# Kernel tuning notes

Hardware: AMD Instinct MI355X
Metric: run time of the kernel (lower is better)

The kernel has to match this reference:

```python
import jax, jax.numpy as jnp
import numpy as np

N, E, ET, C, H, L = 100000, 500000, 3, 128, 128, 3
LN_EPS = 1e-5
L2_EPS = 1e-12


def setup_inputs() -> dict:
    ks = jax.random.split(jax.random.key(0), 12)
    s = 0.05
    return {
        "x": jax.random.normal(ks[0], (N, C), jnp.float32),
        "edges": jax.random.randint(ks[1], (ET, 2, E), 0, N),
        "Wp": jax.random.normal(ks[2], (ET, C, C), jnp.float32) * s,
        "bp": jax.random.normal(ks[3], (ET, C), jnp.float32) * s,
        "Wl0": jax.random.normal(ks[4], (ET, C, H), jnp.float32) * s,
        "bl0": jax.random.normal(ks[5], (ET, H), jnp.float32) * s,
        "Wr0": jax.random.normal(ks[6], (ET, C, H), jnp.float32) * s,
        "Wl": jax.random.normal(ks[7], (L - 1, ET, H, H), jnp.float32) * s,
        "bl": jax.random.normal(ks[8], (L - 1, ET, H), jnp.float32) * s,
        "Wr": jax.random.normal(ks[9], (L - 1, ET, H, H), jnp.float32) * s,
        "ln_g": jnp.ones((L - 1, H), jnp.float32),
        "ln_b": jnp.zeros((L - 1, H), jnp.float32),
    }


def _mean_aggr(msg, dst, n):
    # scatter-mean of per-edge messages onto destination nodes
    summed = jax.ops.segment_sum(msg, dst, num_segments=n)
    deg = jax.ops.segment_sum(jnp.ones((dst.shape[0],), msg.dtype), dst, num_segments=n)
    return summed / jnp.maximum(deg, 1.0)[:, None]


def _sage(h, ei, Wl_, bl_, Wr_, Wp_=None, bp_=None, normalize=False):
    # PyG SAGEConv: out = lin_l(mean_{j in N(i)} h_j) + lin_r(h_i)
    src, dst = ei[0], ei[1]
    hs = jax.nn.relu(h @ Wp_ + bp_) if Wp_ is not None else h  # project=True path
    agg = _mean_aggr(hs[src], dst, h.shape[0])
    out = agg @ Wl_ + bl_ + h @ Wr_
    if normalize:
        out = out / jnp.maximum(jnp.linalg.norm(out, axis=-1, keepdims=True), L2_EPS)
    return out


def _layer_norm(h, g, b):
    mu = h.mean(-1, keepdims=True)
    var = ((h - mu) ** 2).mean(-1, keepdims=True)
    return (h - mu) / jnp.sqrt(var + LN_EPS) * g + b


def _forward(x, edges, Wp, bp, Wl0, bl0, Wr0, Wl, bl, Wr, ln_g, ln_b):
    et = edges.shape[0]
    # layer 0: project=True, normalize=True; HeteroConv mean over edge types
    h = sum(_sage(x, edges[t], Wl0[t], bl0[t], Wr0[t], Wp[t], bp[t], True)
            for t in range(et)) / et
    h = _layer_norm(jax.nn.relu(h), ln_g[0], ln_b[0])  # dropout = identity (eval)
    n_rest = Wl.shape[0]
    for l in range(n_rest):
        h = sum(_sage(h, edges[t], Wl[l, t], bl[l, t], Wr[l, t])
                for t in range(et)) / et
        if l != n_rest - 1:
            h = _layer_norm(jax.nn.relu(h), ln_g[l + 1], ln_b[l + 1])
    return h


def reference(x, edges, Wp, bp, Wl0, bl0, Wr0, Wl, bl, Wr, ln_g, ln_b):
    return _forward(x, edges, Wp, bp, Wl0, bl0, Wr0, Wl, bl, Wr, ln_g, ln_b)
```

## Files before the change

kernel.cpp:

```cpp
#include <hip/hip_runtime.h>
#include <math.h>

#define CH 128
#define ETC 3
#define LN_EPS 1e-5f

typedef unsigned short u16;
typedef unsigned int u32;
typedef __attribute__((ext_vector_type(8))) short short8;
typedef __attribute__((ext_vector_type(4))) float f32x4;

__device__ __forceinline__ u16 f2bf(float f) {
    u32 u = __float_as_uint(f);
    u += 0x7FFFu + ((u >> 16) & 1u);
    return (u16)(u >> 16);
}
__device__ __forceinline__ float bflo(u32 u) { return __uint_as_float(u << 16); }
__device__ __forceinline__ float bfhi(u32 u) { return __uint_as_float(u & 0xFFFF0000u); }

__device__ __forceinline__ f32x4 mfma16(short8 a, short8 b, f32x4 c) {
    return __builtin_amdgcn_mfma_f32_16x16x32_bf16(a, b, c, 0, 0, 0);
}
__device__ __forceinline__ short8 ld8(const u16* p) { return *(const short8*)p; }

__global__ __launch_bounds__(256) void pack_w(
    const float* __restrict__ Wp, const float* __restrict__ Wl0,
    const float* __restrict__ Wr0, const float* __restrict__ Wl,
    const float* __restrict__ Wr, const float* __restrict__ bl,
    u16* __restrict__ Bswz, float* __restrict__ bls)
{
    if (blockIdx.x == 0) {
        int l = threadIdx.x >> 7, i = threadIdx.x & 127;
        bls[threadIdx.x] = (bl[((size_t)l * ETC + 0) * CH + i] +
                            bl[((size_t)l * ETC + 1) * CH + i] +
                            bl[((size_t)l * ETC + 2) * CH + i]) * (1.f / 3.f);
    }
    int grp = blockIdx.x * 256 + threadIdx.x;
    if (grp >= 17 * 2048) return;
    int lane = grp & 63;
    int t1 = grp >> 6;
    int nt = t1 & 7, t2 = t1 >> 3;
    int s = t2 & 3, mat = t2 >> 2;
    int q = lane >> 4, c = lane & 15;
    int nn = nt * 16 + c;

    const float* s0;
    const float* s1 = nullptr;
    const float* s2 = nullptr;
    float scale = 1.f;
    if (mat < 3) {
        s0 = Wp + (size_t)mat * CH * CH;
    } else if (mat < 9) {
        int t = (mat - 3) >> 1;
        s0 = ((mat - 3) & 1) ? Wr0 + (size_t)t * CH * CH : Wl0 + (size_t)t * CH * CH;
    } else {
        int l = (mat < 13) ? 0 : 1;
        int mm = mat - (l ? 13 : 9);
        scale = 1.f / 3.f;
        if (mm < 3) s0 = Wl + ((size_t)l * ETC + mm) * CH * CH;
        else {
            s0 = Wr + ((size_t)l * ETC + 0) * CH * CH;
            s1 = s0 + CH * CH;
            s2 = s1 + CH * CH;
        }
    }
    short8 o;
    #pragma unroll
    for (int j = 0; j < 8; ++j) {
        int k = s * 32 + q * 8 + j;
        float v = s0[(size_t)k * CH + nn];
        if (s1) v += s1[(size_t)k * CH + nn] + s2[(size_t)k * CH + nn];
        o[j] = (short)f2bf(v * scale);
    }
    *(short8*)&Bswz[(size_t)grp * 8] = o;
}

__global__ __launch_bounds__(256) void cast_x(
    const float* __restrict__ x, u16* __restrict__ xb, int total)
{
    int i = (blockIdx.x * 256 + threadIdx.x) * 8;
    if (i >= total) return;
    short8 o;
    #pragma unroll
    for (int j = 0; j < 8; ++j) o[j] = (short)f2bf(x[i + j]);
    *(short8*)&xb[i] = o;
}

template<int MODE>
__global__ __launch_bounds__(256) void combine_k(
    const u16* __restrict__ agg0, const u16* __restrict__ agg1,
    const u16* __restrict__ agg2, const u16* __restrict__ self,
    const u16* __restrict__ Bs, const float* __restrict__ bias,
    const float* __restrict__ lg, const float* __restrict__ lb,
    u16* __restrict__ outb, float* __restrict__ outf, int nrows)
{
    constexpr int RF = 2;
    __shared__ __align__(16) u16 Bsh[CH * CH];
    const int tid = threadIdx.x;
    const int w = tid >> 6, lane = tid & 63;
    const int q = lane >> 4, c = lane & 15;
    const int rbase = (blockIdx.x * 4 + w) * (RF * 16);
    const u16* aggs[3] = {agg0, agg1, agg2};
    constexpr int NM = (MODE == 0) ? 6 : ((MODE == 3) ? 1 : 4);

    f32x4 acc[RF][8] = {};
    f32x4 res[RF][8];
    if constexpr (MODE == 0) {
        #pragma unroll
        for (int rf = 0; rf < RF; ++rf)
            #pragma unroll
            for (int nt = 0; nt < 8; ++nt) res[rf][nt] = (f32x4){0.f, 0.f, 0.f, 0.f};
    }

    #pragma unroll
    for (int m = 0; m < NM; ++m) {
        __syncthreads();
        const u16* bsrc = Bs + (size_t)m * CH * CH;
        #pragma unroll
        for (int i = 0; i < 8; ++i)
            *(short8*)&Bsh[(i * 256 + tid) * 8] = ld8(&bsrc[(i * 256 + tid) * 8]);
        __syncthreads();

        const u16* A;
        if constexpr (MODE == 0)      A = (m & 1) ? self : aggs[m >> 1];
        else if constexpr (MODE == 3) A = self;
        else                          A = (m < 3) ? aggs[m] : self;

        #pragma unroll
        for (int s = 0; s < 4; ++s) {
            short8 af[RF];
            #pragma unroll
            for (int rf = 0; rf < RF; ++rf)
                af[rf] = ld8(&A[(size_t)(rbase + rf * 16 + c) * CH + s * 32 + q * 8]);
            #pragma unroll
            for (int nt = 0; nt < 8; ++nt) {
                short8 bv = *(const short8*)&Bsh[((size_t)(s * 8 + nt) * 64 + lane) * 8];
                #pragma unroll
                for (int rf = 0; rf < RF; ++rf)
                    acc[rf][nt] = mfma16(af[rf], bv, acc[rf][nt]);
            }
        }

        if constexpr (MODE == 0) {
            if (m & 1) {
                const int t = m >> 1;
                #pragma unroll
                for (int rf = 0; rf < RF; ++rf) {
                    float ss[4] = {0.f, 0.f, 0.f, 0.f};
                    #pragma unroll
                    for (int nt = 0; nt < 8; ++nt) {
                        float bf = bias[t * CH + nt * 16 + c];
                        #pragma unroll
                        for (int r = 0; r < 4; ++r) {
                            float v = acc[rf][nt][r] + bf;
                            acc[rf][nt][r] = v;
                            ss[r] += v * v;
                        }
                    }
                    #pragma unroll
                    for (int msk = 1; msk < 16; msk <<= 1)
                        #pragma unroll
                        for (int r = 0; r < 4; ++r) ss[r] += __shfl_xor(ss[r], msk, 64);
                    float sc[4];
                    #pragma unroll
                    for (int r = 0; r < 4; ++r)
                        sc[r] = 1.f / (3.f * fmaxf(sqrtf(ss[r]), 1e-12f));
                    #pragma unroll
                    for (int nt = 0; nt < 8; ++nt)
                        #pragma unroll
                        for (int r = 0; r < 4; ++r) {
                            res[rf][nt][r] += acc[rf][nt][r] * sc[r];
                            acc[rf][nt][r] = 0.f;
                        }
                }
            }
        }
    }

    if constexpr (MODE != 0) {
        #pragma unroll
        for (int nt = 0; nt < 8; ++nt) {
            float bv = bias[nt * 16 + c];
            #pragma unroll
            for (int rf = 0; rf < RF; ++rf)
                #pragma unroll
                for (int r = 0; r < 4; ++r) acc[rf][nt][r] += bv;
        }
    }

    if constexpr (MODE == 2) {
        #pragma unroll
        for (int rf = 0; rf < RF; ++rf)
            #pragma unroll
            for (int nt = 0; nt < 8; ++nt)
                #pragma unroll
                for (int r = 0; r < 4; ++r) {
                    int row = rbase + rf * 16 + q * 4 + r;
                    if (row < nrows) outf[(size_t)row * CH + nt * 16 + c] = acc[rf][nt][r];
                }
        return;
    }

    if constexpr (MODE == 3) {
        #pragma unroll
        for (int rf = 0; rf < RF; ++rf)
            #pragma unroll
            for (int nt = 0; nt < 8; ++nt)
                #pragma unroll
                for (int r = 0; r < 4; ++r) {
                    int row = rbase + rf * 16 + q * 4 + r;
                    outb[(size_t)row * CH + nt * 16 + c] = f2bf(fmaxf(acc[rf][nt][r], 0.f));
                }
        return;
    }

    auto& bank = (MODE == 0) ? res : acc;
    #pragma unroll
    for (int rf = 0; rf < RF; ++rf) {
        float s1[4] = {0.f, 0.f, 0.f, 0.f}, s2[4] = {0.f, 0.f, 0.f, 0.f};
        #pragma unroll
        for (int nt = 0; nt < 8; ++nt)
            #pragma unroll
            for (int r = 0; r < 4; ++r) {
                float v = fmaxf(bank[rf][nt][r], 0.f);
                bank[rf][nt][r] = v;
                s1[r] += v;
                s2[r] += v * v;
            }
        #pragma unroll
        for (int msk = 1; msk < 16; msk <<= 1)
            #pragma unroll
            for (int r = 0; r < 4; ++r) {
                s1[r] += __shfl_xor(s1[r], msk, 64);
                s2[r] += __shfl_xor(s2[r], msk, 64);
            }
        float mu[4], rs[4];
        #pragma unroll
        for (int r = 0; r < 4; ++r) {
            mu[r] = s1[r] * (1.f / 128.f);
            float var = s2[r] * (1.f / 128.f) - mu[r] * mu[r];
            rs[r] = rsqrtf(var + LN_EPS);
        }
        #pragma unroll
        for (int nt = 0; nt < 8; ++nt) {
            float gv = lg[nt * 16 + c], bv = lb[nt * 16 + c];
            #pragma unroll
            for (int r = 0; r < 4; ++r) {
                int row = rbase + rf * 16 + q * 4 + r;
                outb[(size_t)row * CH + nt * 16 + c] =
                    f2bf((bank[rf][nt][r] - mu[r]) * rs[r] * gv + bv);
            }
        }
    }
}

__global__ __launch_bounds__(256) void agg_k(
    const u16* __restrict__ msg, const int* __restrict__ rowptr,
    const int* __restrict__ col, u16* __restrict__ agg, int n,
    int Ecap, unsigned long long aggstride)
{
    const int t = blockIdx.y;
    rowptr += (size_t)t * (n + 1);
    col += (size_t)t * Ecap;
    agg += (size_t)t * aggstride;

    int gid = blockIdx.x * 256 + threadIdx.x;
    int node = gid >> 5;
    int lane = threadIdx.x & 31;
    if (node >= n) return;
    int s = rowptr[node], e = rowptr[node + 1];
    const uint2* m64 = (const uint2*)msg;
    float a0 = 0.f, a1 = 0.f, a2 = 0.f, a3 = 0.f;
    float b0 = 0.f, b1 = 0.f, b2 = 0.f, b3 = 0.f;
    float c0 = 0.f, c1 = 0.f, c2 = 0.f, c3 = 0.f;
    float d0 = 0.f, d1 = 0.f, d2 = 0.f, d3 = 0.f;
    int j = s;
    for (; j + 4 <= e; j += 4) {
        int i0 = col[j], i1 = col[j + 1], i2 = col[j + 2], i3 = col[j + 3];
        uint2 v0 = m64[(size_t)i0 * 32 + lane];
        uint2 v1 = m64[(size_t)i1 * 32 + lane];
        uint2 v2 = m64[(size_t)i2 * 32 + lane];
        uint2 v3 = m64[(size_t)i3 * 32 + lane];
        a0 += bflo(v0.x); a1 += bfhi(v0.x); a2 += bflo(v0.y); a3 += bfhi(v0.y);
        b0 += bflo(v1.x); b1 += bfhi(v1.x); b2 += bflo(v1.y); b3 += bfhi(v1.y);
        c0 += bflo(v2.x); c1 += bfhi(v2.x); c2 += bflo(v2.y); c3 += bfhi(v2.y);
        d0 += bflo(v3.x); d1 += bfhi(v3.x); d2 += bflo(v3.y); d3 += bfhi(v3.y);
    }
    for (; j < e; ++j) {
        int i0 = col[j];
        uint2 v0 = m64[(size_t)i0 * 32 + lane];
        a0 += bflo(v0.x); a1 += bfhi(v0.x); a2 += bflo(v0.y); a3 += bfhi(v0.y);
    }
    a0 += b0 + c0 + d0; a1 += b1 + c1 + d1; a2 += b2 + c2 + d2; a3 += b3 + c3 + d3;
    float inv = 1.f / (float)max(e - s, 1);
    uint2 o;
    o.x = (u32)f2bf(a0 * inv) | ((u32)f2bf(a1 * inv) << 16);
    o.y = (u32)f2bf(a2 * inv) | ((u32)f2bf(a3 * inv) << 16);
    ((uint2*)agg)[(size_t)node * 32 + lane] = o;
}

__global__ __launch_bounds__(256) void hist_k(
    const int* __restrict__ edges, int* __restrict__ cnt, int E, int n)
{
    int t = blockIdx.y;
    int e = blockIdx.x * 256 + threadIdx.x;
    if (e >= E) return;
    int dst = edges[(size_t)t * 2 * E + E + e];
    atomicAdd(&cnt[t * n + dst], 1);
}

__global__ __launch_bounds__(256) void scan1_k(
    const int* __restrict__ cnt, int* __restrict__ bsum, int n, int nbs)
{
    int t = blockIdx.y, b = blockIdx.x;
    int i = b * 256 + threadIdx.x;
    int v = (i < n) ? cnt[t * n + i] : 0;
    #pragma unroll
    for (int m = 1; m < 64; m <<= 1) v += __shfl_xor(v, m, 64);
    __shared__ int wsum[4];
    if ((threadIdx.x & 63) == 0) wsum[threadIdx.x >> 6] = v;
    __syncthreads();
    if (threadIdx.x == 0) bsum[t * nbs + b] = wsum[0] + wsum[1] + wsum[2] + wsum[3];
}

__global__ __launch_bounds__(512) void scan2_k(int* __restrict__ bsum, int nbs, int nb)
{
    int t = blockIdx.x;
    int tid = threadIdx.x;
    __shared__ int sh[512];
    int v = (tid < nb) ? bsum[t * nbs + tid] : 0;
    sh[tid] = v;
    __syncthreads();
    for (int off = 1; off < 512; off <<= 1) {
        int x = (tid >= off) ? sh[tid - off] : 0;
        __syncthreads();
        sh[tid] += x;
        __syncthreads();
    }
    if (tid < nb) bsum[t * nbs + tid] = sh[tid] - v;
}

__global__ __launch_bounds__(256) void scan3_k(
    const int* __restrict__ cnt, const int* __restrict__ bsum,
    int* __restrict__ rowptr, int n, int nbs)
{
    int t = blockIdx.y, b = blockIdx.x;
    int tid = threadIdx.x;
    int i = b * 256 + tid;
    __shared__ int sh[256];
    int v = (i < n) ? cnt[t * n + i] : 0;
    sh[tid] = v;
    __syncthreads();
    for (int off = 1; off < 256; off <<= 1) {
        int x = (tid >= off) ? sh[tid - off] : 0;
        __syncthreads();
        sh[tid] += x;
        __syncthreads();
    }
    int excl = sh[tid] - v + bsum[t * nbs + b];
    if (i < n) rowptr[(size_t)t * (n + 1) + i] = excl;
    if (i == n - 1) rowptr[(size_t)t * (n + 1) + n] = excl + v;
}

__global__ __launch_bounds__(256) void fill_k(
    const int* __restrict__ edges, const int* __restrict__ rowptr,
    int* __restrict__ cnt2, int* __restrict__ colbuf, int E, int n)
{
    int t = blockIdx.y;
    int e = blockIdx.x * 256 + threadIdx.x;
    if (e >= E) return;
    int src = edges[(size_t)t * 2 * E + e];
    int dst = edges[(size_t)t * 2 * E + E + e];
    int pos = rowptr[(size_t)t * (n + 1) + dst] + atomicAdd(&cnt2[t * n + dst], 1);
    colbuf[(size_t)t * E + pos] = src;
}

extern "C" void kernel_launch(void* const* d_in, const int* in_sizes, int n_in,
                              void* d_out, int out_size, void* d_ws, size_t ws_size,
                              hipStream_t stream) {
    const float* x    = (const float*)d_in[0];
    const int*   edges= (const int*)d_in[1];
    const float* Wp   = (const float*)d_in[2];
    const float* bp   = (const float*)d_in[3];
    const float* Wl0  = (const float*)d_in[4];
    const float* bl0  = (const float*)d_in[5];
    const float* Wr0  = (const float*)d_in[6];
    const float* Wl   = (const float*)d_in[7];
    const float* bl   = (const float*)d_in[8];
    const float* Wr   = (const float*)d_in[9];
    const float* ln_g = (const float*)d_in[10];
    const float* ln_b = (const float*)d_in[11];
    float* out = (float*)d_out;

    const int n  = in_sizes[0] / CH;
    const int E  = in_sizes[1] / (2 * ETC);
    const int npad = ((n + 127) / 128) * 128;
    const int NBS = 512;
    const int nb = (n + 255) / 256;
    const size_t MS = (size_t)CH * CH;

    char* p = (char*)d_ws;
    u16* xb   = (u16*)p;  p += (size_t)npad * CH * 2;
    u16* hs   = (u16*)p;  p += (size_t)npad * CH * 2;
    u16* agg  = (u16*)p;  p += (size_t)ETC * npad * CH * 2;
    u16* Bswz = (u16*)p;  p += 17 * MS * 2;
    float* bls = (float*)p; p += 256 * 4;
    int* cnt    = (int*)p;  p += (size_t)ETC * n * 4;
    int* rowptr = (int*)p;  p += (size_t)ETC * (n + 1) * 4;
    int* colbuf = (int*)p;  p += (size_t)ETC * E * 4;
    int* bsum   = (int*)p;

    const dim3 b256(256);
    const dim3 ge((E + 255) / 256, ETC);
    const dim3 gs(nb, ETC);
    const int gb = (n + 127) / 128;
    const int ga = (n * 32 + 255) / 256;

    hipMemsetAsync(cnt, 0, (size_t)ETC * n * sizeof(int), stream);
    hist_k<<<ge, b256, 0, stream>>>(edges, cnt, E, n);
    scan1_k<<<gs, b256, 0, stream>>>(cnt, bsum, n, NBS);
    scan2_k<<<ETC, 512, 0, stream>>>(bsum, NBS, nb);
    scan3_k<<<gs, b256, 0, stream>>>(cnt, bsum, rowptr, n, NBS);
    hipMemsetAsync(cnt, 0, (size_t)ETC * n * sizeof(int), stream);
    fill_k<<<ge, b256, 0, stream>>>(edges, rowptr, cnt, colbuf, E, n);

    pack_w<<<136, b256, 0, stream>>>(Wp, Wl0, Wr0, Wl, Wr, bl, Bswz, bls);
    cast_x<<<(n * CH / 8 + 255) / 256, b256, 0, stream>>>(x, xb, n * CH);

    for (int t = 0; t < ETC; ++t) {
        combine_k<3><<<gb, b256, 0, stream>>>(
            nullptr, nullptr, nullptr, xb, Bswz + (size_t)t * MS, bp + t * CH,
            nullptr, nullptr, hs, nullptr, n);
        agg_k<<<dim3(ga, 1), b256, 0, stream>>>(hs, rowptr + (size_t)t * (n + 1),
                                                colbuf + (size_t)t * E,
                                                agg + (size_t)t * npad * CH, n, 0, 0ull);
    }
    combine_k<0><<<gb, b256, 0, stream>>>(agg, agg + (size_t)npad * CH,
                                          agg + (size_t)2 * npad * CH, xb,
                                          Bswz + 3 * MS, bl0, ln_g, ln_b, hs, nullptr, n);

    agg_k<<<dim3(ga, ETC), b256, 0, stream>>>(hs, rowptr, colbuf, agg, n, E,
                                              (unsigned long long)npad * CH);
    combine_k<1><<<gb, b256, 0, stream>>>(agg, agg + (size_t)npad * CH,
                                          agg + (size_t)2 * npad * CH, hs,
                                          Bswz + 9 * MS, bls, ln_g + CH, ln_b + CH,
                                          hs, nullptr, n);

    agg_k<<<dim3(ga, ETC), b256, 0, stream>>>(hs, rowptr, colbuf, agg, n, E,
                                              (unsigned long long)npad * CH);
    combine_k<2><<<gb, b256, 0, stream>>>(agg, agg + (size_t)npad * CH,
                                          agg + (size_t)2 * npad * CH, hs,
                                          Bswz + 13 * MS, bls + CH, nullptr, nullptr,
                                          nullptr, out, n);
}
```

Measured before the change: 706.2 us.

## Transform node features before aggregation and batch all edge types per launch

Uses the linearity of mean aggregation to apply the per-edge-type lin_l weights before the gather. One GEMM kernel now produces all three transformed projections plus the summed self term into a 512-wide buffer, and a single gather launch aggregates all edge types. Layer 0 also merges the three per-type projection and aggregation passes into batched launches, folds the x cast into the GEMM, and moves bias, LayerNorm and the final sum into a lightweight per-node merge kernel. This cuts kernel launches and separate per-type passes. In exchange it adds a wider intermediate buffer, strided gathers over 1 KB rows, and bf16 rounding before aggregation rather than after.

```diff
diff --git a/kernel.cpp b/kernel.cpp
--- a/kernel.cpp
+++ b/kernel.cpp
@@ -4,6 +4,7 @@
 #define CH 128
 #define ETC 3
 #define LN_EPS 1e-5f
+#define MS (CH * CH)
 
 typedef unsigned short u16;
 typedef unsigned int u32;
@@ -49,19 +50,19 @@
     const float* s2 = nullptr;
     float scale = 1.f;
     if (mat < 3) {
-        s0 = Wp + (size_t)mat * CH * CH;
+        s0 = Wp + (size_t)mat * MS;
     } else if (mat < 9) {
         int t = (mat - 3) >> 1;
-        s0 = ((mat - 3) & 1) ? Wr0 + (size_t)t * CH * CH : Wl0 + (size_t)t * CH * CH;
+        s0 = ((mat - 3) & 1) ? Wr0 + (size_t)t * MS : Wl0 + (size_t)t * MS;
     } else {
         int l = (mat < 13) ? 0 : 1;
         int mm = mat - (l ? 13 : 9);
         scale = 1.f / 3.f;
-        if (mm < 3) s0 = Wl + ((size_t)l * ETC + mm) * CH * CH;
+        if (mm < 3) s0 = Wl + ((size_t)l * ETC + mm) * MS;
         else {
-            s0 = Wr + ((size_t)l * ETC + 0) * CH * CH;
-            s1 = s0 + CH * CH;
-            s2 = s1 + CH * CH;
+            s0 = Wr + ((size_t)l * ETC + 0) * MS;
+            s1 = s0 + MS;
+            s2 = s1 + MS;
         }
     }
     short8 o;
@@ -75,212 +76,191 @@
     *(short8*)&Bswz[(size_t)grp * 8] = o;
 }
 
-__global__ __launch_bounds__(256) void cast_x(
-    const float* __restrict__ x, u16* __restrict__ xb, int total)
-{
-    int i = (blockIdx.x * 256 + threadIdx.x) * 8;
-    if (i >= total) return;
-    short8 o;
-    #pragma unroll
-    for (int j = 0; j < 8; ++j) o[j] = (short)f2bf(x[i + j]);
-    *(short8*)&xb[i] = o;
-}
-
-template<int MODE>
-__global__ __launch_bounds__(256) void combine_k(
-    const u16* __restrict__ agg0, const u16* __restrict__ agg1,
-    const u16* __restrict__ agg2, const u16* __restrict__ self,
-    const u16* __restrict__ Bs, const float* __restrict__ bias,
-    const float* __restrict__ lg, const float* __restrict__ lb,
-    u16* __restrict__ outb, float* __restrict__ outf, int nrows)
-{
-    constexpr int RF = 2;
-    __shared__ __align__(16) u16 Bsh[CH * CH];
+template<int NC, bool AF32, bool BIASRELU>
+__global__ __launch_bounds__(256) void mega_k(
+    const void* __restrict__ Ap, const u16* __restrict__ Bs,
+    const float* __restrict__ bias, u16* __restrict__ out, int nrows)
+{
+    __shared__ __align__(16) u16 Bsh[MS];
     const int tid = threadIdx.x;
     const int w = tid >> 6, lane = tid & 63;
-    const int q = lane >> 4, c = lane & 15;
-    const int rbase = (blockIdx.x * 4 + w) * (RF * 16);
-    const u16* aggs[3] = {agg0, agg1, agg2};
-    constexpr int NM = (MODE == 0) ? 6 : ((MODE == 3) ? 1 : 4);
-
-    f32x4 acc[RF][8] = {};
-    f32x4 res[RF][8];
-    if constexpr (MODE == 0) {
-        #pragma unroll
-        for (int rf = 0; rf < RF; ++rf)
-            #pragma unroll
-            for (int nt = 0; nt < 8; ++nt) res[rf][nt] = (f32x4){0.f, 0.f, 0.f, 0.f};
-    }
-
+    const int q = lane >> 4, cc = lane & 15;
+    const int rbase = (blockIdx.x * 4 + w) * 32;
+
+    short8 af[2][4];
     #pragma unroll
-    for (int m = 0; m < NM; ++m) {
-        __syncthreads();
-        const u16* bsrc = Bs + (size_t)m * CH * CH;
+    for (int rf = 0; rf < 2; ++rf) {
+        int row = rbase + rf * 16 + cc;
+        int rcl = min(row, nrows - 1);
+        #pragma unroll
+        for (int s = 0; s < 4; ++s) {
+            if constexpr (AF32) {
+                const float* xp = (const float*)Ap + (size_t)rcl * CH + s * 32 + q * 8;
+                float4 f0 = *(const float4*)xp;
+                float4 f1 = *(const float4*)(xp + 4);
+                short8 o;
+                o[0] = (short)f2bf(f0.x); o[1] = (short)f2bf(f0.y);
+                o[2] = (short)f2bf(f0.z); o[3] = (short)f2bf(f0.w);
+                o[4] = (short)f2bf(f1.x); o[5] = (short)f2bf(f1.y);
+                o[6] = (short)f2bf(f1.z); o[7] = (short)f2bf(f1.w);
+                af[rf][s] = o;
+            } else {
+                af[rf][s] = ld8((const u16*)Ap + (size_t)rcl * CH + s * 32 + q * 8);
+            }
+        }
+    }
+
+    for (int cb = 0; cb < NC; ++cb) {
+        __syncthreads();
+        const u16* bsrc = Bs + (size_t)cb * MS;
         #pragma unroll
         for (int i = 0; i < 8; ++i)
             *(short8*)&Bsh[(i * 256 + tid) * 8] = ld8(&bsrc[(i * 256 + tid) * 8]);
         __syncthreads();
 
-        const u16* A;
-        if constexpr (MODE == 0)      A = (m & 1) ? self : aggs[m >> 1];
-        else if constexpr (MODE == 3) A = self;
-        else                          A = (m < 3) ? aggs[m] : self;
-
-        #pragma unroll
-        for (int s = 0; s < 4; ++s) {
-            short8 af[RF];
-            #pragma unroll
-            for (int rf = 0; rf < RF; ++rf)
-                af[rf] = ld8(&A[(size_t)(rbase + rf * 16 + c) * CH + s * 32 + q * 8]);
+        f32x4 acc[2][8] = {};
+        #pragma unroll
+        for (int s = 0; s < 4; ++s)
             #pragma unroll
             for (int nt = 0; nt < 8; ++nt) {
                 short8 bv = *(const short8*)&Bsh[((size_t)(s * 8 + nt) * 64 + lane) * 8];
-                #pragma unroll
-                for (int rf = 0; rf < RF; ++rf)
-                    acc[rf][nt] = mfma16(af[rf], bv, acc[rf][nt]);
-            }
-        }
-
-        if constexpr (MODE == 0) {
-            if (m & 1) {
-                const int t = m >> 1;
-                #pragma unroll
-                for (int rf = 0; rf < RF; ++rf) {
-                    float ss[4] = {0.f, 0.f, 0.f, 0.f};
-                    #pragma unroll
-                    for (int nt = 0; nt < 8; ++nt) {
-                        float bf = bias[t * CH + nt * 16 + c];
-                        #pragma unroll
-                        for (int r = 0; r < 4; ++r) {
-                            float v = acc[rf][nt][r] + bf;
-                            acc[rf][nt][r] = v;
-                            ss[r] += v * v;
-                        }
-                    }
-                    #pragma unroll
-                    for (int msk = 1; msk < 16; msk <<= 1)
-                        #pragma unroll
-                        for (int r = 0; r < 4; ++r) ss[r] += __shfl_xor(ss[r], msk, 64);
-                    float sc[4];
-                    #pragma unroll
-                    for (int r = 0; r < 4; ++r)
-                        sc[r] = 1.f / (3.f * fmaxf(sqrtf(ss[r]), 1e-12f));
-                    #pragma unroll
-                    for (int nt = 0; nt < 8; ++nt)
-                        #pragma unroll
-                        for (int r = 0; r < 4; ++r) {
-                            res[rf][nt][r] += acc[rf][nt][r] * sc[r];
-                            acc[rf][nt][r] = 0.f;
-                        }
-                }
-            }
-        }
-    }
-
-    if constexpr (MODE != 0) {
+                acc[0][nt] = mfma16(af[0][s], bv, acc[0][nt]);
+                acc[1][nt] = mfma16(af[1][s], bv, acc[1][nt]);
+            }
+
         #pragma unroll
         for (int nt = 0; nt < 8; ++nt) {
-            float bv = bias[nt * 16 + c];
-            #pragma unroll
-            for (int rf = 0; rf < RF; ++rf)
-                #pragma unroll
-                for (int r = 0; r < 4; ++r) acc[rf][nt][r] += bv;
-        }
-    }
-
-    if constexpr (MODE == 2) {
-        #pragma unroll
-        for (int rf = 0; rf < RF; ++rf)
-            #pragma unroll
-            for (int nt = 0; nt < 8; ++nt)
+            float bb = 0.f;
+            if constexpr (BIASRELU) bb = bias[cb * CH + nt * 16 + cc];
+            #pragma unroll
+            for (int rf = 0; rf < 2; ++rf)
                 #pragma unroll
                 for (int r = 0; r < 4; ++r) {
                     int row = rbase + rf * 16 + q * 4 + r;
-                    if (row < nrows) outf[(size_t)row * CH + nt * 16 + c] = acc[rf][nt][r];
+                    float v = acc[rf][nt][r] + bb;
+                    if constexpr (BIASRELU) v = fmaxf(v, 0.f);
+                    out[(size_t)row * 512 + cb * CH + nt * 16 + cc] = f2bf(v);
                 }
-        return;
-    }
-
-    if constexpr (MODE == 3) {
-        #pragma unroll
-        for (int rf = 0; rf < RF; ++rf)
-            #pragma unroll
-            for (int nt = 0; nt < 8; ++nt)
+        }
+    }
+}
+
+__global__ __launch_bounds__(256) void gemm0b_k(
+    const u16* __restrict__ aggm, const float* __restrict__ x,
+    const u16* __restrict__ Bswz, const float* __restrict__ bl0,
+    u16* __restrict__ normed, int nrows, int npad)
+{
+    __shared__ __align__(16) u16 Bsh[MS];
+    const int t = blockIdx.y;
+    const int tid = threadIdx.x;
+    const int w = tid >> 6, lane = tid & 63;
+    const int q = lane >> 4, cc = lane & 15;
+    const int rbase = (blockIdx.x * 4 + w) * 32;
+    const u16* A0 = aggm + (size_t)t * npad * CH;
+
+    f32x4 acc[2][8] = {};
+    for (int m = 0; m < 2; ++m) {
+        __syncthreads();
+        const u16* bsrc = Bswz + (size_t)(3 + 2 * t + m) * MS;
+        #pragma unroll
+        for (int i = 0; i < 8; ++i)
+            *(short8*)&Bsh[(i * 256 + tid) * 8] = ld8(&bsrc[(i * 256 + tid) * 8]);
+        __syncthreads();
+
+        short8 af[2][4];
+        #pragma unroll
+        for (int rf = 0; rf < 2; ++rf) {
+            int row = rbase + rf * 16 + cc;
+            if (m == 0) {
                 #pragma unroll
-                for (int r = 0; r < 4; ++r) {
-                    int row = rbase + rf * 16 + q * 4 + r;
-                    outb[(size_t)row * CH + nt * 16 + c] = f2bf(fmaxf(acc[rf][nt][r], 0.f));
+                for (int s = 0; s < 4; ++s)
+                    af[rf][s] = ld8(&A0[(size_t)row * CH + s * 32 + q * 8]);
+            } else {
+                int rcl = min(row, nrows - 1);
+                #pragma unroll
+                for (int s = 0; s < 4; ++s) {
+                    const float* xp = x + (size_t)rcl * CH + s * 32 + q * 8;
+                    float4 f0 = *(const float4*)xp;
+                    float4 f1 = *(const float4*)(xp + 4);
+                    short8 o;
+                    o[0] = (short)f2bf(f0.x); o[1] = (short)f2bf(f0.y);
+                    o[2] = (short)f2bf(f0.z); o[3] = (short)f2bf(f0.w);
+                    o[4] = (short)f2bf(f1.x); o[5] = (short)f2bf(f1.y);
+                    o[6] = (short)f2bf(f1.z); o[7] = (short)f2bf(f1.w);
+                    af[rf][s] = o;
                 }
-        return;
-    }
-
-    auto& bank = (MODE == 0) ? res : acc;
+            }
+        }
+        #pragma unroll
+        for (int s = 0; s < 4; ++s)
+            #pragma unroll
+            for (int nt = 0; nt < 8; ++nt) {
+                short8 bv = *(const short8*)&Bsh[((size_t)(s * 8 + nt) * 64 + lane) * 8];
+                acc[0][nt] = mfma16(af[0][s], bv, acc[0][nt]);
+                acc[1][nt] = mfma16(af[1][s], bv, acc[1][nt]);
+            }
+    }
+
+    u16* outp = normed + (size_t)t * npad * CH;
     #pragma unroll
-    for (int rf = 0; rf < RF; ++rf) {
-        float s1[4] = {0.f, 0.f, 0.f, 0.f}, s2[4] = {0.f, 0.f, 0.f, 0.f};
+    for (int rf = 0; rf < 2; ++rf) {
+        float ss[4] = {0.f, 0.f, 0.f, 0.f};
+        #pragma unroll
+        for (int nt = 0; nt < 8; ++nt) {
+            float bf = bl0[t * CH + nt * 16 + cc];
+            #pragma unroll
+            for (int r = 0; r < 4; ++r) {
+                float v = acc[rf][nt][r] + bf;
+                acc[rf][nt][r] = v;
+                ss[r] += v * v;
+            }
+        }
+        #pragma unroll
+        for (int msk = 1; msk < 16; msk <<= 1)
+            #pragma unroll
+            for (int r = 0; r < 4; ++r) ss[r] += __shfl_xor(ss[r], msk, 64);
+        float sc[4];
+        #pragma unroll
+        for (int r = 0; r < 4; ++r)
+            sc[r] = 1.f / (3.f * fmaxf(sqrtf(ss[r]), 1e-12f));
         #pragma unroll
         for (int nt = 0; nt < 8; ++nt)
-            #pragma unroll
-            for (int r = 0; r < 4; ++r) {
-                float v = fmaxf(bank[rf][nt][r], 0.f);
-                bank[rf][nt][r] = v;
-                s1[r] += v;
-                s2[r] += v * v;
-            }
-        #pragma unroll
-        for (int msk = 1; msk < 16; msk <<= 1)
-            #pragma unroll
-            for (int r = 0; r < 4; ++r) {
-                s1[r] += __shfl_xor(s1[r], msk, 64);
-                s2[r] += __shfl_xor(s2[r], msk, 64);
-            }
-        float mu[4], rs[4];
-        #pragma unroll
-        for (int r = 0; r < 4; ++r) {
-            mu[r] = s1[r] * (1.f / 128.f);
-            float var = s2[r] * (1.f / 128.f) - mu[r] * mu[r];
-            rs[r] = rsqrtf(var + LN_EPS);
-        }
-        #pragma unroll
-        for (int nt = 0; nt < 8; ++nt) {
-            float gv = lg[nt * 16 + c], bv = lb[nt * 16 + c];
             #pragma unroll
             for (int r = 0; r < 4; ++r) {
                 int row = rbase + rf * 16 + q * 4 + r;
-                outb[(size_t)row * CH + nt * 16 + c] =
-                    f2bf((bank[rf][nt][r] - mu[r]) * rs[r] * gv + bv);
-            }
-        }
-    }
-}
-
-__global__ __launch_bounds__(256) void agg_k(
-    const u16* __restrict__ msg, const int* __restrict__ rowptr,
-    const int* __restrict__ col, u16* __restrict__ agg, int n,
-    int Ecap, unsigned long long aggstride)
+                outp[(size_t)row * CH + nt * 16 + cc] = f2bf(acc[rf][nt][r] * sc[r]);
+            }
+    }
+}
+
+__global__ __launch_bounds__(256) void agg3_k(
+    const u16* __restrict__ mega, const int* __restrict__ rowptr,
+    const int* __restrict__ col, u16* __restrict__ dst, int n,
+    int Ecap, unsigned long long dststride)
 {
     const int t = blockIdx.y;
     rowptr += (size_t)t * (n + 1);
     col += (size_t)t * Ecap;
-    agg += (size_t)t * aggstride;
+    const u16* src = mega + (size_t)t * CH;
+    dst += (size_t)t * dststride;
 
     int gid = blockIdx.x * 256 + threadIdx.x;
     int node = gid >> 5;
     int lane = threadIdx.x & 31;
     if (node >= n) return;
     int s = rowptr[node], e = rowptr[node + 1];
-    const uint2* m64 = (const uint2*)msg;
     float a0 = 0.f, a1 = 0.f, a2 = 0.f, a3 = 0.f;
     float b0 = 0.f, b1 = 0.f, b2 = 0.f, b3 = 0.f;
     float c0 = 0.f, c1 = 0.f, c2 = 0.f, c3 = 0.f;
     float d0 = 0.f, d1 = 0.f, d2 = 0.f, d3 = 0.f;
     int j = s;
+    const int lo = lane * 4;
     for (; j + 4 <= e; j += 4) {
         int i0 = col[j], i1 = col[j + 1], i2 = col[j + 2], i3 = col[j + 3];
-        uint2 v0 = m64[(size_t)i0 * 32 + lane];
-        uint2 v1 = m64[(size_t)i1 * 32 + lane];
-        uint2 v2 = m64[(size_t)i2 * 32 + lane];
-        uint2 v3 = m64[(size_t)i3 * 32 + lane];
+        uint2 v0 = *(const uint2*)&src[(size_t)i0 * 512 + lo];
+        uint2 v1 = *(const uint2*)&src[(size_t)i1 * 512 + lo];
+        uint2 v2 = *(const uint2*)&src[(size_t)i2 * 512 + lo];
+        uint2 v3 = *(const uint2*)&src[(size_t)i3 * 512 + lo];
         a0 += bflo(v0.x); a1 += bfhi(v0.x); a2 += bflo(v0.y); a3 += bfhi(v0.y);
         b0 += bflo(v1.x); b1 += bfhi(v1.x); b2 += bflo(v1.y); b3 += bfhi(v1.y);
         c0 += bflo(v2.x); c1 += bfhi(v2.x); c2 += bflo(v2.y); c3 += bfhi(v2.y);
@@ -288,7 +268,7 @@
     }
     for (; j < e; ++j) {
         int i0 = col[j];
-        uint2 v0 = m64[(size_t)i0 * 32 + lane];
+        uint2 v0 = *(const uint2*)&src[(size_t)i0 * 512 + lo];
         a0 += bflo(v0.x); a1 += bfhi(v0.x); a2 += bflo(v0.y); a3 += bfhi(v0.y);
     }
     a0 += b0 + c0 + d0; a1 += b1 + c1 + d1; a2 += b2 + c2 + d2; a3 += b3 + c3 + d3;
@@ -296,7 +276,62 @@
     uint2 o;
     o.x = (u32)f2bf(a0 * inv) | ((u32)f2bf(a1 * inv) << 16);
     o.y = (u32)f2bf(a2 * inv) | ((u32)f2bf(a3 * inv) << 16);
-    ((uint2*)agg)[(size_t)node * 32 + lane] = o;
+    *(uint2*)&dst[(size_t)node * CH + lo] = o;
+}
+
+template<int MODE>
+__global__ __launch_bounds__(256) void merge_k(
+    const u16* __restrict__ a0, const u16* __restrict__ a1,
+    const u16* __restrict__ a2, const u16* __restrict__ zm,
+    const float* __restrict__ bias, const float* __restrict__ lg,
+    const float* __restrict__ lb, u16* __restrict__ outb,
+    float* __restrict__ outf, int n)
+{
+    int gid = blockIdx.x * 256 + threadIdx.x;
+    int node = gid >> 5;
+    int lane = threadIdx.x & 31;
+    if (node >= n) return;
+    const int lo = lane * 4;
+    uint2 u0 = *(const uint2*)&a0[(size_t)node * CH + lo];
+    uint2 u1 = *(const uint2*)&a1[(size_t)node * CH + lo];
+    uint2 u2 = *(const uint2*)&a2[(size_t)node * CH + lo];
+    float v0 = bflo(u0.x) + bflo(u1.x) + bflo(u2.x);
+    float v1 = bfhi(u0.x) + bfhi(u1.x) + bfhi(u2.x);
+    float v2 = bflo(u0.y) + bflo(u1.y) + bflo(u2.y);
+    float v3 = bfhi(u0.y) + bfhi(u1.y) + bfhi(u2.y);
+    if constexpr (MODE >= 1) {
+        uint2 uz = *(const uint2*)&zm[(size_t)node * 512 + 384 + lo];
+        float4 bb = *(const float4*)&bias[lo];
+        v0 += bflo(uz.x) + bb.x;
+        v1 += bfhi(uz.x) + bb.y;
+        v2 += bflo(uz.y) + bb.z;
+        v3 += bfhi(uz.y) + bb.w;
+    }
+    if constexpr (MODE == 2) {
+        float4 o = make_float4(v0, v1, v2, v3);
+        *(float4*)&outf[(size_t)node * CH + lo] = o;
+        return;
+    }
+    v0 = fmaxf(v0, 0.f); v1 = fmaxf(v1, 0.f);
+    v2 = fmaxf(v2, 0.f); v3 = fmaxf(v3, 0.f);
+    float s1 = v0 + v1 + v2 + v3;
+    float s2 = v0 * v0 + v1 * v1 + v2 * v2 + v3 * v3;
+    #pragma unroll
+    for (int m = 1; m < 32; m <<= 1) {
+        s1 += __shfl_xor(s1, m, 64);
+        s2 += __shfl_xor(s2, m, 64);
+    }
+    float mu = s1 * (1.f / 128.f);
+    float var = s2 * (1.f / 128.f) - mu * mu;
+    float rstd = rsqrtf(var + LN_EPS);
+    float4 g = *(const float4*)&lg[lo];
+    float4 b = *(const float4*)&lb[lo];
+    uint2 o;
+    o.x = (u32)f2bf((v0 - mu) * rstd * g.x + b.x) |
+          ((u32)f2bf((v1 - mu) * rstd * g.y + b.y) << 16);
+    o.y = (u32)f2bf((v2 - mu) * rstd * g.z + b.z) |
+          ((u32)f2bf((v3 - mu) * rstd * g.w + b.w) << 16);
+    *(uint2*)&outb[(size_t)node * CH + lo] = o;
 }
 
 __global__ __launch_bounds__(256) void hist_k(
@@ -397,13 +432,12 @@
     const int npad = ((n + 127) / 128) * 128;
     const int NBS = 512;
     const int nb = (n + 255) / 256;
-    const size_t MS = (size_t)CH * CH;
 
     char* p = (char*)d_ws;
-    u16* xb   = (u16*)p;  p += (size_t)npad * CH * 2;
     u16* hs   = (u16*)p;  p += (size_t)npad * CH * 2;
-    u16* agg  = (u16*)p;  p += (size_t)ETC * npad * CH * 2;
-    u16* Bswz = (u16*)p;  p += 17 * MS * 2;
+    u16* mega = (u16*)p;  p += (size_t)npad * 512 * 2;
+    u16* aggm = (u16*)p;  p += (size_t)ETC * npad * CH * 2;
+    u16* Bswz = (u16*)p;  p += 17 * (size_t)MS * 2;
     float* bls = (float*)p; p += 256 * 4;
     int* cnt    = (int*)p;  p += (size_t)ETC * n * 4;
     int* rowptr = (int*)p;  p += (size_t)ETC * (n + 1) * 4;
@@ -413,8 +447,9 @@
     const dim3 b256(256);
     const dim3 ge((E + 255) / 256, ETC);
     const dim3 gs(nb, ETC);
-    const int gb = (n + 127) / 128;
+    const int gb = npad / 128;
     const int ga = (n * 32 + 255) / 256;
+    const unsigned long long astr = (unsigned long long)npad * CH;
 
     hipMemsetAsync(cnt, 0, (size_t)ETC * n * sizeof(int), stream);
     hist_k<<<ge, b256, 0, stream>>>(edges, cnt, E, n);
@@ -425,31 +460,22 @@
     fill_k<<<ge, b256, 0, stream>>>(edges, rowptr, cnt, colbuf, E, n);
 
     pack_w<<<136, b256, 0, stream>>>(Wp, Wl0, Wr0, Wl, Wr, bl, Bswz, bls);
-    cast_x<<<(n * CH / 8 + 255) / 256, b256, 0, stream>>>(x, xb, n * CH);
-
-    for (int t = 0; t < ETC; ++t) {
-        combine_k<3><<<gb, b256, 0, stream>>>(
-            nullptr, nullptr, nullptr, xb, Bswz + (size_t)t * MS, bp + t * CH,
-            nullptr, nullptr, hs, nullptr, n);
-        agg_k<<<dim3(ga, 1), b256, 0, stream>>>(hs, rowptr + (size_t)t * (n + 1),
-                                                colbuf + (size_t)t * E,
-                                                agg + (size_t)t * npad * CH, n, 0, 0ull);
-    }
-    combine_k<0><<<gb, b256, 0, stream>>>(agg, agg + (size_t)npad * CH,
-                                          agg + (size_t)2 * npad * CH, xb,
-                                          Bswz + 3 * MS, bl0, ln_g, ln_b, hs, nullptr, n);
-
-    agg_k<<<dim3(ga, ETC), b256, 0, stream>>>(hs, rowptr, colbuf, agg, n, E,
-                                              (unsigned long long)npad * CH);
-    combine_k<1><<<gb, b256, 0, stream>>>(agg, agg + (size_t)npad * CH,
-                                          agg + (size_t)2 * npad * CH, hs,
-                                          Bswz + 9 * MS, bls, ln_g + CH, ln_b + CH,
-                                          hs, nullptr, n);
-
-    agg_k<<<dim3(ga, ETC), b256, 0, stream>>>(hs, rowptr, colbuf, agg, n, E,
-                                              (unsigned long long)npad * CH);
-    combine_k<2><<<gb, b256, 0, stream>>>(agg, agg + (size_t)npad * CH,
-                                          agg + (size_t)2 * npad * CH, hs,
-                                          Bswz + 13 * MS, bls + CH, nullptr, nullptr,
-                                          nullptr, out, n);
-}
+
+    mega_k<3, true, true><<<gb, b256, 0, stream>>>(x, Bswz, bp, mega, n);
+    agg3_k<<<dim3(ga, ETC), b256, 0, stream>>>(mega, rowptr, colbuf, aggm, n, E, astr);
+    gemm0b_k<<<dim3(gb, ETC), b256, 0, stream>>>(aggm, x, Bswz, bl0, mega, n, npad);
+    merge_k<0><<<ga, b256, 0, stream>>>(mega, mega + astr, mega + 2 * astr,
+                                        nullptr, nullptr, ln_g, ln_b, hs, nullptr, n);
+
+    mega_k<4, false, false><<<gb, b256, 0, stream>>>(hs, Bswz + 9 * (size_t)MS,
+                                                     nullptr, mega, n);
+    agg3_k<<<dim3(ga, ETC), b256, 0, stream>>>(mega, rowptr, colbuf, aggm, n, E, astr);
+    merge_k<1><<<ga, b256, 0, stream>>>(aggm, aggm + astr, aggm + 2 * astr,
+                                        mega, bls, ln_g + CH, ln_b + CH, hs, nullptr, n);
+
+    mega_k<4, false, false><<<gb, b256, 0, stream>>>(hs, Bswz + 13 * (size_t)MS,
+                                                     nullptr, mega, n);
+    agg3_k<<<dim3(ga, ETC), b256, 0, stream>>>(mega, rowptr, colbuf, aggm, n, E, astr);
+    merge_k<2><<<ga, b256, 0, stream>>>(aggm, aggm + astr, aggm + 2 * astr,
+                                        mega, bls + CH, nullptr, nullptr, nullptr, out, n);
+}
```

After: 720.8 us. +2.1%, slower.
